# Optimization experiments

Hardware: AMD Instinct MI355X
Metric: run time of the kernel (lower is better)

The kernel has to match this reference:

```python
import jax, jax.numpy as jnp
import numpy as np

B, V, K, D, E, NE = 32, 512, 16, 128, 32, 8192


def setup_inputs() -> dict:
    key = jax.random.key(0)
    ks = jax.random.split(key, 12)
    s = 0.05
    return {
        "vertex_features": jax.random.normal(ks[0], (B, V, D), jnp.float32),
        "atom_adj": jax.random.randint(ks[1], (B * V * K,), 0, B * V),
        "bond_adj": jax.random.randint(ks[2], (B * V * K,), 0, B * NE),
        "h0": jax.random.normal(ks[3], (B, V, D), jnp.float32),
        "lamda": jnp.full((1,), 0.5, jnp.float32),
        "alpha": jnp.full((1,), 0.1, jnp.float32),
        "l": 1,
        "edge_initial": jax.random.normal(ks[4], (B, NE, E), jnp.float32),
        "vertex_mask": jnp.ones((B, V), jnp.float32),
        "nbs_mask": jax.random.uniform(ks[5], (B, V, K), jnp.float32),
        # label_U1: (D+E) -> D ; label_U2: 2D -> D ; feature_updating: D -> D (variant=False)
        "W1": jax.random.normal(ks[6], (D, D + E), jnp.float32) * s,
        "b1": jax.random.normal(ks[7], (D,), jnp.float32) * s,
        "W2": jax.random.normal(ks[8], (D, 2 * D), jnp.float32) * s,
        "b2": jax.random.normal(ks[9], (D,), jnp.float32) * s,
        "W3": jax.random.normal(ks[10], (D, D), jnp.float32) * s,
        "b3": jax.random.normal(ks[11], (D,), jnp.float32) * s,
    }


def reference(vertex_features, atom_adj, bond_adj, h0, lamda, alpha, l,
              edge_initial, vertex_mask, nbs_mask, W1, b1, W2, b2, W3, b3):
    b, v = vertex_mask.shape
    k = nbs_mask.shape[2]
    d = vertex_features.shape[-1]
    e = edge_initial.shape[-1]
    # gather neighbor vertex and edge features (flat index, torch.index_select semantics)
    vn = vertex_features.reshape(-1, d)[atom_adj].reshape(b, v, k, d)
    en = edge_initial.reshape(-1, e)[bond_adj].reshape(b, v, k, e)
    l_neighbor = jnp.concatenate([vn, en], axis=-1)            # [b,v,k,d+e]
    nl = jax.nn.gelu(l_neighbor @ W1.T + b1, approximate=False)  # exact GELU like torch F.gelu
    nl = jnp.sum(nl * nbs_mask[..., None], axis=-2)            # masked sum over neighbors -> [b,v,d]
    hi = jnp.concatenate([nl, vertex_features], axis=-1) @ W2.T + b2
    theta = jnp.log(lamda / l + 1.0)                           # broadcast scalar (shape [1])
    support = (1.0 - alpha) * hi + alpha * h0                  # variant=False: r == support
    out = theta * (support @ W3.T + b3) + (1.0 - theta) * support
    out = out + vertex_features                                # residual=True
    return out
```

## Files before the change

### kernel.cpp

```cpp
#include <hip/hip_runtime.h>
#include <hip/hip_bf16.h>
#include <math.h>

#define NLSTR 136
#define ASTR  168

typedef __bf16 bf16x8 __attribute__((ext_vector_type(8)));
typedef float f32x4 __attribute__((ext_vector_type(4)));
typedef float f32x16 __attribute__((ext_vector_type(16)));
typedef unsigned short ushort8v __attribute__((ext_vector_type(8)));

union FragU { ushort8v u; bf16x8 b; };

static __device__ inline unsigned short f2bf(float f){
  unsigned u = __float_as_uint(f);
  u += 0x7fffu + ((u >> 16) & 1u);
  return (unsigned short)(u >> 16);
}
static __device__ inline float bf2f(unsigned short u){
  return __uint_as_float(((unsigned)u) << 16);
}
static __device__ inline unsigned pk2(float a, float b){
  union { __hip_bfloat162 h; unsigned u; } r;
  r.h = __float22bfloat162_rn(float2{a, b});
  return r.u;
}
static __device__ inline ushort8v pkcvt8(float4 a, float4 b){
  union { unsigned u[4]; ushort8v v; } r;
  r.u[0] = pk2(a.x, a.y); r.u[1] = pk2(a.z, a.w);
  r.u[2] = pk2(b.x, b.y); r.u[3] = pk2(b.z, b.w);
  return r.v;
}

static __device__ inline float gelu_f(float x){
  float u = x * x;
  float p = fmaf(u, 0.07135481283f, 1.5957691216f);
  float t = x * p;
  float e = __builtin_amdgcn_exp2f(t * -1.44269504f);
  return x * __builtin_amdgcn_rcpf(1.0f + e);
}

__global__ __launch_bounds__(256) void prep_kernel(
    const float* __restrict__ vf, const float* __restrict__ W1,
    const float* __restrict__ W2, const float* __restrict__ W3,
    unsigned short* __restrict__ vfbf, unsigned short* __restrict__ w1f,
    unsigned short* __restrict__ w2f, unsigned short* __restrict__ w3f)
{
  int t = blockIdx.x * 256 + threadIdx.x;
  if (t < 262144){
    const float4* src = (const float4*)vf;
    float4 x = src[t * 2], y = src[t * 2 + 1];
    *(ushort8v*)(vfbf + t * 8) = pkcvt8(x, y);
    return;
  }
  int t2 = t - 262144;
  const float* s;
  unsigned short* d;
  if (t2 < 2560){
    int fragid = t2 >> 6, lane = t2 & 63;
    int nc2 = fragid / 10, kc = fragid % 10, n = lane & 31, h = lane >> 5;
    s = W1 + (nc2 * 32 + n) * 160 + kc * 16 + h * 8;
    d = w1f + t2 * 8;
  } else if (t2 < 6656){
    int t3 = t2 - 2560;
    int fragid = t3 >> 6, lane = t3 & 63;
    int kc = fragid >> 3, nc = fragid & 7, col = lane & 15, quad = lane >> 4;
    s = W2 + (nc * 16 + col) * 256 + kc * 32 + quad * 8;
    d = w2f + t3 * 8;
  } else if (t2 < 8704){
    int t3 = t2 - 6656;
    int fragid = t3 >> 6, lane = t3 & 63;
    int kc = fragid >> 3, nc = fragid & 7, col = lane & 15, quad = lane >> 4;
    s = W3 + (nc * 16 + col) * 128 + kc * 32 + quad * 8;
    d = w3f + t3 * 8;
  } else return;
#pragma unroll
  for (int j = 0; j < 8; j++) d[j] = f2bf(s[j]);
}

__global__ __launch_bounds__(256) void fused_kernel(
    const unsigned short* __restrict__ vfbf,
    const int* __restrict__ aadj, const int* __restrict__ badj,
    const float* __restrict__ edge, const float* __restrict__ nbs,
    const float* __restrict__ h0,
    const unsigned short* __restrict__ w1f, const unsigned short* __restrict__ w2f,
    const unsigned short* __restrict__ w3f,
    const float* __restrict__ b1, const float* __restrict__ b2, const float* __restrict__ b3,
    const float* __restrict__ lamda, const float* __restrict__ alpha,
    const int* __restrict__ lval,
    float* __restrict__ out)
{
  __shared__ __align__(16) unsigned short abuf[2][32 * ASTR];
  __shared__ __align__(16) unsigned short nl_lds[16 * NLSTR];
  __shared__ __align__(16) unsigned short sup_lds[16 * NLSTR];
  const int wid  = threadIdx.x >> 6;
  const int lane = threadIdx.x & 63;
  const int n32  = lane & 31;
  const int h    = lane >> 5;
  const int col  = lane & 15;
  const int quad = lane >> 4;
  const int v0   = blockIdx.x * 16;

  FragU bw[10];
#pragma unroll
  for (int kc = 0; kc < 10; kc++)
    bw[kc].u = *(const ushort8v*)(w1f + ((wid * 10 + kc) * 64 + lane) * 8);

  const float bb1 = b1[wid * 32 + n32];
  const float4* nbs4 = (const float4*)nbs;

  const int srow = threadIdx.x >> 3;
  const int ssub = threadIdx.x & 7;

  ushort8v sv0, sv1; float4 se;
  {
    const int vtx = v0 + (srow >> 4), nb = srow & 15;
    const int a = aadj[vtx * 16 + nb], e = badj[vtx * 16 + nb];
    const ushort8v* vs = (const ushort8v*)(vfbf + (size_t)a * 128 + ssub * 16);
    sv0 = vs[0]; sv1 = vs[1];
    se = *(const float4*)(edge + (size_t)e * 32 + ssub * 4);
  }
  {
    unsigned short* dst = abuf[0] + srow * ASTR + ssub * 16;
    *(ushort8v*)dst = sv0; *(ushort8v*)(dst + 8) = sv1;
    unsigned* ed = (unsigned*)(abuf[0] + srow * ASTR + 128 + ssub * 4);
    ed[0] = pk2(se.x, se.y); ed[1] = pk2(se.z, se.w);
  }

#pragma unroll 1
  for (int p = 0; p < 8; ++p){
    __syncthreads();
    if (p < 7){
      const int vtx = v0 + 2 * (p + 1) + (srow >> 4), nb = srow & 15;
      const int a = aadj[vtx * 16 + nb], e = badj[vtx * 16 + nb];
      const ushort8v* vs = (const ushort8v*)(vfbf + (size_t)a * 128 + ssub * 16);
      sv0 = vs[0]; sv1 = vs[1];
      se = *(const float4*)(edge + (size_t)e * 32 + ssub * 4);
    }

    const unsigned short* ab = abuf[p & 1] + n32 * ASTR + h * 8;
    f32x16 acc = {};
#pragma unroll
    for (int kc = 0; kc < 10; kc++){
      FragU fa;
      fa.u = *(const ushort8v*)(ab + kc * 16);
      acc = __builtin_amdgcn_mfma_f32_32x32x16_bf16(fa.b, bw[kc].b, acc, 0, 0, 0);
    }

    {
      const int vA = v0 + 2 * p;
      const float4 mAlo = nbs4[vA * 4 + h],       mAhi = nbs4[vA * 4 + 2 + h];
      const float4 mBlo = nbs4[(vA + 1) * 4 + h], mBhi = nbs4[(vA + 1) * 4 + 2 + h];
      float sA = gelu_f(acc[0] + bb1) * mAlo.x + gelu_f(acc[1] + bb1) * mAlo.y
               + gelu_f(acc[2] + bb1) * mAlo.z + gelu_f(acc[3] + bb1) * mAlo.w
               + gelu_f(acc[4] + bb1) * mAhi.x + gelu_f(acc[5] + bb1) * mAhi.y
               + gelu_f(acc[6] + bb1) * mAhi.z + gelu_f(acc[7] + bb1) * mAhi.w;
      float sB = gelu_f(acc[8] + bb1) * mBlo.x + gelu_f(acc[9] + bb1) * mBlo.y
               + gelu_f(acc[10] + bb1) * mBlo.z + gelu_f(acc[11] + bb1) * mBlo.w
               + gelu_f(acc[12] + bb1) * mBhi.x + gelu_f(acc[13] + bb1) * mBhi.y
               + gelu_f(acc[14] + bb1) * mBhi.z + gelu_f(acc[15] + bb1) * mBhi.w;
      sA += __shfl_xor(sA, 32, 64);
      sB += __shfl_xor(sB, 32, 64);
      if (h == 0) nl_lds[(2 * p)     * NLSTR + wid * 32 + n32] = f2bf(sA);
      else        nl_lds[(2 * p + 1) * NLSTR + wid * 32 + n32] = f2bf(sB);
    }

    if (p < 7){
      unsigned short* dst = abuf[(p + 1) & 1] + srow * ASTR + ssub * 16;
      *(ushort8v*)dst = sv0; *(ushort8v*)(dst + 8) = sv1;
      unsigned* ed = (unsigned*)(abuf[(p + 1) & 1] + srow * ASTR + 128 + ssub * 4);
      ed[0] = pk2(se.x, se.y); ed[1] = pk2(se.z, se.w);
    }
  }
  __syncthreads();

  const int nc0 = 2 * wid;
  const float th = logf(lamda[0] / (float)lval[0] + 1.0f);
  const float al = alpha[0];

  f32x4 acc2[2] = {};
#pragma unroll
  for (int kc = 0; kc < 8; kc++){
    FragU a;
    if (kc < 4) a.u = *(const ushort8v*)(nl_lds + col * NLSTR + kc * 32 + quad * 8);
    else        a.u = *(const ushort8v*)(vfbf + (size_t)(v0 + col) * 128 + (kc - 4) * 32 + quad * 8);
#pragma unroll
    for (int pq = 0; pq < 2; pq++){
      FragU bf_;
      bf_.u = *(const ushort8v*)(w2f + ((kc * 8 + nc0 + pq) * 64 + lane) * 8);
      acc2[pq] = __builtin_amdgcn_mfma_f32_16x16x32_bf16(a.b, bf_.b, acc2[pq], 0, 0, 0);
    }
  }

  float sup[2][4];
#pragma unroll
  for (int pq = 0; pq < 2; pq++){
    const int d = (nc0 + pq) * 16 + col;
    const float bb = b2[d];
#pragma unroll
    for (int r = 0; r < 4; r++){
      const int vtx = v0 + quad * 4 + r;
      float hi = acc2[pq][r] + bb;
      float s = (1.f - al) * hi + al * h0[vtx * 128 + d];
      sup[pq][r] = s;
      sup_lds[(quad * 4 + r) * NLSTR + d] = f2bf(s);
    }
  }
  __syncthreads();

  f32x4 acc3[2] = {};
#pragma unroll
  for (int kc = 0; kc < 4; kc++){
    FragU a;
    a.u = *(const ushort8v*)(sup_lds + col * NLSTR + kc * 32 + quad * 8);
#pragma unroll
    for (int pq = 0; pq < 2; pq++){
      FragU bf_;
      bf_.u = *(const ushort8v*)(w3f + ((kc * 8 + nc0 + pq) * 64 + lane) * 8);
      acc3[pq] = __builtin_amdgcn_mfma_f32_16x16x32_bf16(a.b, bf_.b, acc3[pq], 0, 0, 0);
    }
  }

#pragma unroll
  for (int pq = 0; pq < 2; pq++){
    const int d = (nc0 + pq) * 16 + col;
    const float bb = b3[d];
#pragma unroll
    for (int r = 0; r < 4; r++){
      const int vtx = v0 + quad * 4 + r;
      float res = bf2f(vfbf[(size_t)vtx * 128 + d]);
      out[vtx * 128 + d] = th * (acc3[pq][r] + bb) + (1.f - th) * sup[pq][r] + res;
    }
  }
}

extern "C" void kernel_launch(void* const* d_in, const int* in_sizes, int n_in,
                              void* d_out, int out_size, void* d_ws, size_t ws_size,
                              hipStream_t stream)
{
  const float* vfp  = (const float*)d_in[0];
  const int*   aadj = (const int*)d_in[1];
  const int*   badj = (const int*)d_in[2];
  const float* h0   = (const float*)d_in[3];
  const float* lam  = (const float*)d_in[4];
  const float* alp  = (const float*)d_in[5];
  const int*   lv   = (const int*)d_in[6];
  const float* edge = (const float*)d_in[7];
  const float* nbs  = (const float*)d_in[9];
  const float* W1   = (const float*)d_in[10];
  const float* b1   = (const float*)d_in[11];
  const float* W2   = (const float*)d_in[12];
  const float* b2   = (const float*)d_in[13];
  const float* W3   = (const float*)d_in[14];
  const float* b3   = (const float*)d_in[15];
  float* out = (float*)d_out;

  unsigned short* w1f  = (unsigned short*)d_ws;
  unsigned short* w2f  = w1f + 20480;
  unsigned short* w3f  = w2f + 32768;
  unsigned short* vfbf = w3f + 16384;

  prep_kernel<<<1058, 256, 0, stream>>>(vfp, W1, W2, W3, vfbf, w1f, w2f, w3f);
  fused_kernel<<<1024, 256, 0, stream>>>(vfbf, aadj, badj, edge, nbs, h0,
                                         w1f, w2f, w3f, b1, b2, b3, lam, alp, lv, out);
}
```

Before: 147.3 us.

## Gather neighbor features directly into registers, one wave per vertex group

Removes the shared-memory staging buffer for gathered neighbor rows. Each wave now loads its own vertices' neighbor vertex and edge features straight into MFMA A-fragments with a register double buffer, and computes all 128 output columns using 16x16x32 MFMAs. The W1 fragments are re-laid out to match. This drops the block-wide syncs and LDS writes from the first stage, but each wave now keeps 32 weight fragments in registers and reloads the edge-part weights from global memory every iteration. The launch bound requests two blocks per CU, which caps register use.

```diff
diff --git a/kernel.cpp b/kernel.cpp
--- a/kernel.cpp
+++ b/kernel.cpp
@@ -3,11 +3,9 @@
 #include <math.h>
 
 #define NLSTR 136
-#define ASTR  168
 
 typedef __bf16 bf16x8 __attribute__((ext_vector_type(8)));
 typedef float f32x4 __attribute__((ext_vector_type(4)));
-typedef float f32x16 __attribute__((ext_vector_type(16)));
 typedef unsigned short ushort8v __attribute__((ext_vector_type(8)));
 
 union FragU { ushort8v u; bf16x8 b; };
@@ -58,8 +56,8 @@
   unsigned short* d;
   if (t2 < 2560){
     int fragid = t2 >> 6, lane = t2 & 63;
-    int nc2 = fragid / 10, kc = fragid % 10, n = lane & 31, h = lane >> 5;
-    s = W1 + (nc2 * 32 + n) * 160 + kc * 16 + h * 8;
+    int kc = fragid >> 3, nc = fragid & 7, col = lane & 15, quad = lane >> 4;
+    s = W1 + (nc * 16 + col) * 160 + kc * 32 + quad * 8;
     d = w1f + t2 * 8;
   } else if (t2 < 6656){
     int t3 = t2 - 2560;
@@ -78,7 +76,7 @@
   for (int j = 0; j < 8; j++) d[j] = f2bf(s[j]);
 }
 
-__global__ __launch_bounds__(256) void fused_kernel(
+__global__ __launch_bounds__(256, 2) void fused_kernel(
     const unsigned short* __restrict__ vfbf,
     const int* __restrict__ aadj, const int* __restrict__ badj,
     const float* __restrict__ edge, const float* __restrict__ nbs,
@@ -90,87 +88,89 @@
     const int* __restrict__ lval,
     float* __restrict__ out)
 {
-  __shared__ __align__(16) unsigned short abuf[2][32 * ASTR];
   __shared__ __align__(16) unsigned short nl_lds[16 * NLSTR];
   __shared__ __align__(16) unsigned short sup_lds[16 * NLSTR];
   const int wid  = threadIdx.x >> 6;
   const int lane = threadIdx.x & 63;
-  const int n32  = lane & 31;
-  const int h    = lane >> 5;
   const int col  = lane & 15;
   const int quad = lane >> 4;
   const int v0   = blockIdx.x * 16;
 
-  FragU bw[10];
-#pragma unroll
-  for (int kc = 0; kc < 10; kc++)
-    bw[kc].u = *(const ushort8v*)(w1f + ((wid * 10 + kc) * 64 + lane) * 8);
-
-  const float bb1 = b1[wid * 32 + n32];
+  FragU bw[32];
+#pragma unroll
+  for (int f = 0; f < 32; f++)
+    bw[f].u = *(const ushort8v*)(w1f + (f * 64 + lane) * 8);
+
+  float b1v[8];
+#pragma unroll
+  for (int nc = 0; nc < 8; nc++) b1v[nc] = b1[nc * 16 + col];
+
+  int a_[4], e_[4];
+#pragma unroll
+  for (int v = 0; v < 4; v++){
+    a_[v] = aadj[(v0 + wid * 4 + v) * 16 + col];
+    e_[v] = badj[(v0 + wid * 4 + v) * 16 + col];
+  }
+
   const float4* nbs4 = (const float4*)nbs;
 
-  const int srow = threadIdx.x >> 3;
-  const int ssub = threadIdx.x & 7;
-
-  ushort8v sv0, sv1; float4 se;
+  ushort8v pav[2][4];
+  FragU    pef[2];
+
   {
-    const int vtx = v0 + (srow >> 4), nb = srow & 15;
-    const int a = aadj[vtx * 16 + nb], e = badj[vtx * 16 + nb];
-    const ushort8v* vs = (const ushort8v*)(vfbf + (size_t)a * 128 + ssub * 16);
-    sv0 = vs[0]; sv1 = vs[1];
-    se = *(const float4*)(edge + (size_t)e * 32 + ssub * 4);
-  }
-  {
-    unsigned short* dst = abuf[0] + srow * ASTR + ssub * 16;
-    *(ushort8v*)dst = sv0; *(ushort8v*)(dst + 8) = sv1;
-    unsigned* ed = (unsigned*)(abuf[0] + srow * ASTR + 128 + ssub * 4);
-    ed[0] = pk2(se.x, se.y); ed[1] = pk2(se.z, se.w);
-  }
-
-#pragma unroll 1
-  for (int p = 0; p < 8; ++p){
-    __syncthreads();
-    if (p < 7){
-      const int vtx = v0 + 2 * (p + 1) + (srow >> 4), nb = srow & 15;
-      const int a = aadj[vtx * 16 + nb], e = badj[vtx * 16 + nb];
-      const ushort8v* vs = (const ushort8v*)(vfbf + (size_t)a * 128 + ssub * 16);
-      sv0 = vs[0]; sv1 = vs[1];
-      se = *(const float4*)(edge + (size_t)e * 32 + ssub * 4);
-    }
-
-    const unsigned short* ab = abuf[p & 1] + n32 * ASTR + h * 8;
-    f32x16 acc = {};
-#pragma unroll
-    for (int kc = 0; kc < 10; kc++){
-      FragU fa;
-      fa.u = *(const ushort8v*)(ab + kc * 16);
-      acc = __builtin_amdgcn_mfma_f32_32x32x16_bf16(fa.b, bw[kc].b, acc, 0, 0, 0);
+    const unsigned short* r = vfbf + (size_t)a_[0] * 128 + quad * 8;
+#pragma unroll
+    for (int kc = 0; kc < 4; kc++) pav[0][kc] = *(const ushort8v*)(r + kc * 32);
+    float4 p0 = *(const float4*)(edge + (size_t)e_[0] * 32 + quad * 8);
+    float4 p1 = *(const float4*)(edge + (size_t)e_[0] * 32 + quad * 8 + 4);
+    pef[0].u = pkcvt8(p0, p1);
+  }
+
+#pragma unroll
+  for (int it = 0; it < 4; ++it){
+    const int cur = it & 1, nxt = cur ^ 1;
+    float4 pe0, pe1;
+    if (it < 3){
+      const unsigned short* r = vfbf + (size_t)a_[it + 1] * 128 + quad * 8;
+#pragma unroll
+      for (int kc = 0; kc < 4; kc++) pav[nxt][kc] = *(const ushort8v*)(r + kc * 32);
+      pe0 = *(const float4*)(edge + (size_t)e_[it + 1] * 32 + quad * 8);
+      pe1 = *(const float4*)(edge + (size_t)e_[it + 1] * 32 + quad * 8 + 4);
+    }
+
+    f32x4 acc[8] = {};
+#pragma unroll
+    for (int kc = 0; kc < 4; kc++){
+      FragU fa; fa.u = pav[cur][kc];
+#pragma unroll
+      for (int nc = 0; nc < 8; nc++)
+        acc[nc] = __builtin_amdgcn_mfma_f32_16x16x32_bf16(fa.b, bw[kc * 8 + nc].b, acc[nc], 0, 0, 0);
+    }
+#pragma unroll
+    for (int nc = 0; nc < 8; nc++){
+      FragU bf_;
+      bf_.u = *(const ushort8v*)(w1f + ((32 + nc) * 64 + lane) * 8);
+      acc[nc] = __builtin_amdgcn_mfma_f32_16x16x32_bf16(pef[cur].b, bf_.b, acc[nc], 0, 0, 0);
     }
 
     {
-      const int vA = v0 + 2 * p;
-      const float4 mAlo = nbs4[vA * 4 + h],       mAhi = nbs4[vA * 4 + 2 + h];
-      const float4 mBlo = nbs4[(vA + 1) * 4 + h], mBhi = nbs4[(vA + 1) * 4 + 2 + h];
-      float sA = gelu_f(acc[0] + bb1) * mAlo.x + gelu_f(acc[1] + bb1) * mAlo.y
-               + gelu_f(acc[2] + bb1) * mAlo.z + gelu_f(acc[3] + bb1) * mAlo.w
-               + gelu_f(acc[4] + bb1) * mAhi.x + gelu_f(acc[5] + bb1) * mAhi.y
-               + gelu_f(acc[6] + bb1) * mAhi.z + gelu_f(acc[7] + bb1) * mAhi.w;
-      float sB = gelu_f(acc[8] + bb1) * mBlo.x + gelu_f(acc[9] + bb1) * mBlo.y
-               + gelu_f(acc[10] + bb1) * mBlo.z + gelu_f(acc[11] + bb1) * mBlo.w
-               + gelu_f(acc[12] + bb1) * mBhi.x + gelu_f(acc[13] + bb1) * mBhi.y
-               + gelu_f(acc[14] + bb1) * mBhi.z + gelu_f(acc[15] + bb1) * mBhi.w;
-      sA += __shfl_xor(sA, 32, 64);
-      sB += __shfl_xor(sB, 32, 64);
-      if (h == 0) nl_lds[(2 * p)     * NLSTR + wid * 32 + n32] = f2bf(sA);
-      else        nl_lds[(2 * p + 1) * NLSTR + wid * 32 + n32] = f2bf(sB);
-    }
-
-    if (p < 7){
-      unsigned short* dst = abuf[(p + 1) & 1] + srow * ASTR + ssub * 16;
-      *(ushort8v*)dst = sv0; *(ushort8v*)(dst + 8) = sv1;
-      unsigned* ed = (unsigned*)(abuf[(p + 1) & 1] + srow * ASTR + 128 + ssub * 4);
-      ed[0] = pk2(se.x, se.y); ed[1] = pk2(se.z, se.w);
-    }
+      const int vtx = v0 + wid * 4 + it;
+      const float4 mk = nbs4[vtx * 4 + quad];
+#pragma unroll
+      for (int nc = 0; nc < 8; nc++){
+        float g0 = gelu_f(acc[nc][0] + b1v[nc]);
+        float g1 = gelu_f(acc[nc][1] + b1v[nc]);
+        float g2 = gelu_f(acc[nc][2] + b1v[nc]);
+        float g3 = gelu_f(acc[nc][3] + b1v[nc]);
+        float s  = g0 * mk.x + g1 * mk.y + g2 * mk.z + g3 * mk.w;
+        s += __shfl_xor(s, 16, 64);
+        s += __shfl_xor(s, 32, 64);
+        if ((nc >> 1) == quad)
+          nl_lds[(wid * 4 + it) * NLSTR + nc * 16 + col] = f2bf(s);
+      }
+    }
+
+    if (it < 3) pef[nxt].u = pkcvt8(pe0, pe1);
   }
   __syncthreads();
 
```

Result: slower. 154.2 us (+4.7%).

## Gather MFMA A-fragments directly into registers, dropping LDS staging buffer

Applied to the files above, without the earlier changes.

Each wave now gathers its own neighbor vertex and edge rows straight from global memory into registers in MFMA fragment layout, double-buffered across iterations. This removes the shared abuf staging, the per-iteration __syncthreads, and the LDS write/read round trip. In exchange the four waves each redundantly load the same gathered rows, register pressure rises sharply, and launch_bounds is set to one block per SM. The main loop is also fully unrolled.

```diff
diff --git a/kernel.cpp b/kernel.cpp
--- a/kernel.cpp
+++ b/kernel.cpp
@@ -3,7 +3,6 @@
 #include <math.h>
 
 #define NLSTR 136
-#define ASTR  168
 
 typedef __bf16 bf16x8 __attribute__((ext_vector_type(8)));
 typedef float f32x4 __attribute__((ext_vector_type(4)));
@@ -78,7 +77,7 @@
   for (int j = 0; j < 8; j++) d[j] = f2bf(s[j]);
 }
 
-__global__ __launch_bounds__(256) void fused_kernel(
+__global__ __launch_bounds__(256, 1) void fused_kernel(
     const unsigned short* __restrict__ vfbf,
     const int* __restrict__ aadj, const int* __restrict__ badj,
     const float* __restrict__ edge, const float* __restrict__ nbs,
@@ -90,7 +89,6 @@
     const int* __restrict__ lval,
     float* __restrict__ out)
 {
-  __shared__ __align__(16) unsigned short abuf[2][32 * ASTR];
   __shared__ __align__(16) unsigned short nl_lds[16 * NLSTR];
   __shared__ __align__(16) unsigned short sup_lds[16 * NLSTR];
   const int wid  = threadIdx.x >> 6;
@@ -107,50 +105,59 @@
     bw[kc].u = *(const ushort8v*)(w1f + ((wid * 10 + kc) * 64 + lane) * 8);
 
   const float bb1 = b1[wid * 32 + n32];
-  const float4* nbs4 = (const float4*)nbs;
-
-  const int srow = threadIdx.x >> 3;
-  const int ssub = threadIdx.x & 7;
-
-  ushort8v sv0, sv1; float4 se;
+  const float4* nbs4 = (const float4*)(nbs);
+
+  int a_[8], e_[8];
   {
-    const int vtx = v0 + (srow >> 4), nb = srow & 15;
-    const int a = aadj[vtx * 16 + nb], e = badj[vtx * 16 + nb];
-    const ushort8v* vs = (const ushort8v*)(vfbf + (size_t)a * 128 + ssub * 16);
-    sv0 = vs[0]; sv1 = vs[1];
-    se = *(const float4*)(edge + (size_t)e * 32 + ssub * 4);
-  }
+    const int base = v0 * 16 + n32;
+#pragma unroll
+    for (int p = 0; p < 8; p++){
+      a_[p] = aadj[base + 32 * p];
+      e_[p] = badj[base + 32 * p];
+    }
+  }
+
+  ushort8v pav[2][8];
+  float4   pe[2][4];
+
   {
-    unsigned short* dst = abuf[0] + srow * ASTR + ssub * 16;
-    *(ushort8v*)dst = sv0; *(ushort8v*)(dst + 8) = sv1;
-    unsigned* ed = (unsigned*)(abuf[0] + srow * ASTR + 128 + ssub * 4);
-    ed[0] = pk2(se.x, se.y); ed[1] = pk2(se.z, se.w);
-  }
-
-#pragma unroll 1
+    const unsigned short* vr = vfbf + (size_t)a_[0] * 128 + h * 8;
+#pragma unroll
+    for (int kc = 0; kc < 8; kc++) pav[0][kc] = *(const ushort8v*)(vr + kc * 16);
+    const float* er = edge + (size_t)e_[0] * 32 + h * 8;
+    pe[0][0] = *(const float4*)(er);      pe[0][1] = *(const float4*)(er + 4);
+    pe[0][2] = *(const float4*)(er + 16); pe[0][3] = *(const float4*)(er + 20);
+  }
+
+#pragma unroll
   for (int p = 0; p < 8; ++p){
-    __syncthreads();
+    const int cur = p & 1, nxt = cur ^ 1;
     if (p < 7){
-      const int vtx = v0 + 2 * (p + 1) + (srow >> 4), nb = srow & 15;
-      const int a = aadj[vtx * 16 + nb], e = badj[vtx * 16 + nb];
-      const ushort8v* vs = (const ushort8v*)(vfbf + (size_t)a * 128 + ssub * 16);
-      sv0 = vs[0]; sv1 = vs[1];
-      se = *(const float4*)(edge + (size_t)e * 32 + ssub * 4);
-    }
-
-    const unsigned short* ab = abuf[p & 1] + n32 * ASTR + h * 8;
+      const unsigned short* vr = vfbf + (size_t)a_[p + 1] * 128 + h * 8;
+#pragma unroll
+      for (int kc = 0; kc < 8; kc++) pav[nxt][kc] = *(const ushort8v*)(vr + kc * 16);
+      const float* er = edge + (size_t)e_[p + 1] * 32 + h * 8;
+      pe[nxt][0] = *(const float4*)(er);      pe[nxt][1] = *(const float4*)(er + 4);
+      pe[nxt][2] = *(const float4*)(er + 16); pe[nxt][3] = *(const float4*)(er + 20);
+    }
+
+    const int vA = v0 + 2 * p;
+    const float4 mAlo = nbs4[vA * 4 + h],       mAhi = nbs4[vA * 4 + 2 + h];
+    const float4 mBlo = nbs4[(vA + 1) * 4 + h], mBhi = nbs4[(vA + 1) * 4 + 2 + h];
+
+    FragU ef0, ef1;
+    ef0.u = pkcvt8(pe[cur][0], pe[cur][1]);
+    ef1.u = pkcvt8(pe[cur][2], pe[cur][3]);
     f32x16 acc = {};
 #pragma unroll
-    for (int kc = 0; kc < 10; kc++){
-      FragU fa;
-      fa.u = *(const ushort8v*)(ab + kc * 16);
+    for (int kc = 0; kc < 8; kc++){
+      FragU fa; fa.u = pav[cur][kc];
       acc = __builtin_amdgcn_mfma_f32_32x32x16_bf16(fa.b, bw[kc].b, acc, 0, 0, 0);
     }
+    acc = __builtin_amdgcn_mfma_f32_32x32x16_bf16(ef0.b, bw[8].b, acc, 0, 0, 0);
+    acc = __builtin_amdgcn_mfma_f32_32x32x16_bf16(ef1.b, bw[9].b, acc, 0, 0, 0);
 
     {
-      const int vA = v0 + 2 * p;
-      const float4 mAlo = nbs4[vA * 4 + h],       mAhi = nbs4[vA * 4 + 2 + h];
-      const float4 mBlo = nbs4[(vA + 1) * 4 + h], mBhi = nbs4[(vA + 1) * 4 + 2 + h];
       float sA = gelu_f(acc[0] + bb1) * mAlo.x + gelu_f(acc[1] + bb1) * mAlo.y
                + gelu_f(acc[2] + bb1) * mAlo.z + gelu_f(acc[3] + bb1) * mAlo.w
                + gelu_f(acc[4] + bb1) * mAhi.x + gelu_f(acc[5] + bb1) * mAhi.y
@@ -163,13 +170,6 @@
       sB += __shfl_xor(sB, 32, 64);
       if (h == 0) nl_lds[(2 * p)     * NLSTR + wid * 32 + n32] = f2bf(sA);
       else        nl_lds[(2 * p + 1) * NLSTR + wid * 32 + n32] = f2bf(sB);
-    }
-
-    if (p < 7){
-      unsigned short* dst = abuf[(p + 1) & 1] + srow * ASTR + ssub * 16;
-      *(ushort8v*)dst = sv0; *(ushort8v*)(dst + 8) = sv1;
-      unsigned* ed = (unsigned*)(abuf[(p + 1) & 1] + srow * ASTR + 128 + ssub * 4);
-      ed[0] = pk2(se.x, se.y); ed[1] = pk2(se.z, se.w);
     }
   }
   __syncthreads();
```

Measured after the change: 166.4 us. 13.0% more time.

## Pre-convert edge features to bf16 and deepen gather pipeline to 64-row stages

Applied to the files above, without the earlier changes.

The prep kernel now converts the whole edge feature tensor to bf16, so the fused kernel gathers half-width edge rows. The fused kernel also loads all neighbour indices up front and stages 64 gathered rows per buffer, using wider per-thread loads. Each stage runs two MFMA blocks, and the next stage's gather is issued two iterations ahead. The aim is to hide gather latency and cut gathered bytes. The cost is a full extra read and write of the edge tensor on every call.

```diff
diff --git a/kernel.cpp b/kernel.cpp
--- a/kernel.cpp
+++ b/kernel.cpp
@@ -41,16 +41,24 @@
 }
 
 __global__ __launch_bounds__(256) void prep_kernel(
-    const float* __restrict__ vf, const float* __restrict__ W1,
-    const float* __restrict__ W2, const float* __restrict__ W3,
-    unsigned short* __restrict__ vfbf, unsigned short* __restrict__ w1f,
-    unsigned short* __restrict__ w2f, unsigned short* __restrict__ w3f)
+    const float* __restrict__ vf, const float* __restrict__ edge,
+    const float* __restrict__ W1, const float* __restrict__ W2, const float* __restrict__ W3,
+    unsigned short* __restrict__ vfbf, unsigned short* __restrict__ ebf,
+    unsigned short* __restrict__ w1f, unsigned short* __restrict__ w2f,
+    unsigned short* __restrict__ w3f)
 {
   int t = blockIdx.x * 256 + threadIdx.x;
+  if (t < 1048576){
+    const float4* src = (const float4*)edge;
+    float4 x = src[t * 2], y = src[t * 2 + 1];
+    *(ushort8v*)(ebf + (size_t)t * 8) = pkcvt8(x, y);
+    return;
+  }
+  t -= 1048576;
   if (t < 262144){
     const float4* src = (const float4*)vf;
     float4 x = src[t * 2], y = src[t * 2 + 1];
-    *(ushort8v*)(vfbf + t * 8) = pkcvt8(x, y);
+    *(ushort8v*)(vfbf + (size_t)t * 8) = pkcvt8(x, y);
     return;
   }
   int t2 = t - 262144;
@@ -81,7 +89,7 @@
 __global__ __launch_bounds__(256) void fused_kernel(
     const unsigned short* __restrict__ vfbf,
     const int* __restrict__ aadj, const int* __restrict__ badj,
-    const float* __restrict__ edge, const float* __restrict__ nbs,
+    const unsigned short* __restrict__ ebf, const float* __restrict__ nbs,
     const float* __restrict__ h0,
     const unsigned short* __restrict__ w1f, const unsigned short* __restrict__ w2f,
     const unsigned short* __restrict__ w3f,
@@ -90,7 +98,7 @@
     const int* __restrict__ lval,
     float* __restrict__ out)
 {
-  __shared__ __align__(16) unsigned short abuf[2][32 * ASTR];
+  __shared__ __align__(16) unsigned short abuf[2][64 * ASTR];
   __shared__ __align__(16) unsigned short nl_lds[16 * NLSTR];
   __shared__ __align__(16) unsigned short sup_lds[16 * NLSTR];
   const int wid  = threadIdx.x >> 6;
@@ -109,46 +117,48 @@
   const float bb1 = b1[wid * 32 + n32];
   const float4* nbs4 = (const float4*)nbs;
 
-  const int srow = threadIdx.x >> 3;
-  const int ssub = threadIdx.x & 7;
-
-  ushort8v sv0, sv1; float4 se;
-  {
-    const int vtx = v0 + (srow >> 4), nb = srow & 15;
-    const int a = aadj[vtx * 16 + nb], e = badj[vtx * 16 + nb];
-    const ushort8v* vs = (const ushort8v*)(vfbf + (size_t)a * 128 + ssub * 16);
-    sv0 = vs[0]; sv1 = vs[1];
-    se = *(const float4*)(edge + (size_t)e * 32 + ssub * 4);
-  }
-  {
-    unsigned short* dst = abuf[0] + srow * ASTR + ssub * 16;
-    *(ushort8v*)dst = sv0; *(ushort8v*)(dst + 8) = sv1;
-    unsigned* ed = (unsigned*)(abuf[0] + srow * ASTR + 128 + ssub * 4);
-    ed[0] = pk2(se.x, se.y); ed[1] = pk2(se.z, se.w);
-  }
+  const int srow = threadIdx.x >> 2;
+  const int ssub = threadIdx.x & 3;
+
+  int a_[4], e_[4];
+#pragma unroll
+  for (int q = 0; q < 4; q++){
+    const int fi = v0 * 16 + q * 64 + srow;
+    a_[q] = aadj[fi];
+    e_[q] = badj[fi];
+  }
+
+  ushort8v pv0, pv1, pv2, pv3, pe1;
+
+#define ISSUE(q) { \
+    const ushort8v* vr = (const ushort8v*)(vfbf + (size_t)a_[q] * 128) + ssub * 4; \
+    pv0 = vr[0]; pv1 = vr[1]; pv2 = vr[2]; pv3 = vr[3]; \
+    pe1 = *(const ushort8v*)(ebf + (size_t)e_[q] * 32 + ssub * 8); }
+#define COMMIT(bsel) { \
+    unsigned short* dst = abuf[bsel] + srow * ASTR + ssub * 32; \
+    *(ushort8v*)(dst)      = pv0; *(ushort8v*)(dst + 8)  = pv1; \
+    *(ushort8v*)(dst + 16) = pv2; *(ushort8v*)(dst + 24) = pv3; \
+    *(ushort8v*)(abuf[bsel] + srow * ASTR + 128 + ssub * 8) = pe1; }
+
+  ISSUE(0); COMMIT(0); ISSUE(1);
 
 #pragma unroll 1
-  for (int p = 0; p < 8; ++p){
+  for (int it = 0; it < 4; ++it){
     __syncthreads();
-    if (p < 7){
-      const int vtx = v0 + 2 * (p + 1) + (srow >> 4), nb = srow & 15;
-      const int a = aadj[vtx * 16 + nb], e = badj[vtx * 16 + nb];
-      const ushort8v* vs = (const ushort8v*)(vfbf + (size_t)a * 128 + ssub * 16);
-      sv0 = vs[0]; sv1 = vs[1];
-      se = *(const float4*)(edge + (size_t)e * 32 + ssub * 4);
-    }
-
-    const unsigned short* ab = abuf[p & 1] + n32 * ASTR + h * 8;
-    f32x16 acc = {};
-#pragma unroll
-    for (int kc = 0; kc < 10; kc++){
-      FragU fa;
-      fa.u = *(const ushort8v*)(ab + kc * 16);
-      acc = __builtin_amdgcn_mfma_f32_32x32x16_bf16(fa.b, bw[kc].b, acc, 0, 0, 0);
-    }
-
-    {
-      const int vA = v0 + 2 * p;
+    if (it < 3) COMMIT((it + 1) & 1);
+    if (it < 2) ISSUE(it + 2);
+
+#pragma unroll
+    for (int m = 0; m < 2; m++){
+      const unsigned short* ab = abuf[it & 1] + (m * 32 + n32) * ASTR + h * 8;
+      f32x16 acc = {};
+#pragma unroll
+      for (int kc = 0; kc < 10; kc++){
+        FragU fa;
+        fa.u = *(const ushort8v*)(ab + kc * 16);
+        acc = __builtin_amdgcn_mfma_f32_32x32x16_bf16(fa.b, bw[kc].b, acc, 0, 0, 0);
+      }
+      const int vA = v0 + 4 * it + 2 * m;
       const float4 mAlo = nbs4[vA * 4 + h],       mAhi = nbs4[vA * 4 + 2 + h];
       const float4 mBlo = nbs4[(vA + 1) * 4 + h], mBhi = nbs4[(vA + 1) * 4 + 2 + h];
       float sA = gelu_f(acc[0] + bb1) * mAlo.x + gelu_f(acc[1] + bb1) * mAlo.y
@@ -161,17 +171,12 @@
                + gelu_f(acc[14] + bb1) * mBhi.z + gelu_f(acc[15] + bb1) * mBhi.w;
       sA += __shfl_xor(sA, 32, 64);
       sB += __shfl_xor(sB, 32, 64);
-      if (h == 0) nl_lds[(2 * p)     * NLSTR + wid * 32 + n32] = f2bf(sA);
-      else        nl_lds[(2 * p + 1) * NLSTR + wid * 32 + n32] = f2bf(sB);
-    }
-
-    if (p < 7){
-      unsigned short* dst = abuf[(p + 1) & 1] + srow * ASTR + ssub * 16;
-      *(ushort8v*)dst = sv0; *(ushort8v*)(dst + 8) = sv1;
-      unsigned* ed = (unsigned*)(abuf[(p + 1) & 1] + srow * ASTR + 128 + ssub * 4);
-      ed[0] = pk2(se.x, se.y); ed[1] = pk2(se.z, se.w);
-    }
-  }
+      if (h == 0) nl_lds[(4 * it + 2 * m)     * NLSTR + wid * 32 + n32] = f2bf(sA);
+      else        nl_lds[(4 * it + 2 * m + 1) * NLSTR + wid * 32 + n32] = f2bf(sB);
+    }
+  }
+#undef ISSUE
+#undef COMMIT
   __syncthreads();
 
   const int nc0 = 2 * wid;
@@ -259,8 +264,9 @@
   unsigned short* w2f  = w1f + 20480;
   unsigned short* w3f  = w2f + 32768;
   unsigned short* vfbf = w3f + 16384;
-
-  prep_kernel<<<1058, 256, 0, stream>>>(vfp, W1, W2, W3, vfbf, w1f, w2f, w3f);
-  fused_kernel<<<1024, 256, 0, stream>>>(vfbf, aadj, badj, edge, nbs, h0,
+  unsigned short* ebf  = vfbf + 2097152;
+
+  prep_kernel<<<5154, 256, 0, stream>>>(vfp, edge, W1, W2, W3, vfbf, ebf, w1f, w2f, w3f);
+  fused_kernel<<<1024, 256, 0, stream>>>(vfbf, aadj, badj, ebf, nbs, h0,
                                          w1f, w2f, w3f, b1, b2, b3, lam, alp, lv, out);
 }
```

Result: no change. 146.2 us (-0.7%).
